# Performance work log

Hardware: AMD Instinct MI355X
Metric: run time of the kernel (lower is better)

The kernel has to match this reference:

```python
import jax, jax.numpy as jnp
import numpy as np

B = 8192        # number of drug-cell pairs (graphs)
NPG = 32        # nodes per graph
EPG = 64        # directed edges per graph
N = B * NPG     # total nodes
E = B * EPG     # total edges
CELL = 908      # cell_inp_dim
BN_EPS = 1e-5


def _bn(x):
    # BatchNorm1d in training mode with gamma=1, beta=0 (fresh init), biased var
    m = x.mean(0)
    v = x.var(0)
    return (x - m) * jax.lax.rsqrt(v + BN_EPS)


def _lin_params(k, fan_in, fan_out):
    kw, _ = jax.random.split(k)
    w = jax.random.normal(kw, (fan_in, fan_out), jnp.float32) / np.sqrt(fan_in)
    b = jnp.zeros((fan_out,), jnp.float32)
    return w, b


_DIMS = [("ce_1", CELL, 516), ("ce_2", 516, 256), ("ce_3", 256, 128),
         ("g1_1", 9, 128), ("g1_2", 128, 128),
         ("g2_1", 128, 128), ("g2_2", 128, 128),
         ("d_1", 128, 128), ("d_2", 128, 128),
         ("f_1", 256, 128), ("f_2", 128, 64), ("f_3", 64, 1)]


def setup_inputs() -> dict:
    key = jax.random.key(0)
    ks = jax.random.split(key, 4 + len(_DIMS))
    inp = {}
    inp["cell"] = jax.random.normal(ks[0], (B, CELL), jnp.float32)
    inp["drug_x"] = jax.random.normal(ks[1], (N, 9), jnp.float32)
    g = jnp.arange(E) // EPG  # graph id per edge
    src = g * NPG + jax.random.randint(ks[2], (E,), 0, NPG)
    dst = g * NPG + jax.random.randint(ks[3], (E,), 0, NPG)
    inp["drug_edge_index"] = jnp.stack([src, dst]).astype(jnp.int32)
    inp["drug_batch"] = (jnp.arange(N) // NPG).astype(jnp.int32)
    for i, (nm, a, b) in enumerate(_DIMS):
        w, bb = _lin_params(ks[4 + i], a, b)
        inp[nm + "_w"] = w
        inp[nm + "_b"] = bb
    return inp


def _forward(cell, drug_x, src, dst, batch,
             ce_1_w, ce_1_b, ce_2_w, ce_2_b, ce_3_w, ce_3_b,
             g1_1_w, g1_1_b, g1_2_w, g1_2_b,
             g2_1_w, g2_1_b, g2_2_w, g2_2_b,
             d_1_w, d_1_b, d_2_w, d_2_b,
             f_1_w, f_1_b, f_2_w, f_2_b, f_3_w, f_3_b):
    # cell_emb branch (dropout = identity in eval/reference)
    c = jax.nn.relu(_bn(cell @ ce_1_w + ce_1_b))
    c = jax.nn.relu(_bn(c @ ce_2_w + ce_2_b))
    c = jax.nn.relu(_bn(c @ ce_3_w + ce_3_b))

    # GINConv 1: h = MLP((1+eps)*x + sum_{j in N(i)} x_j), eps=0
    agg = jax.ops.segment_sum(drug_x[src], dst, num_segments=N)
    h = drug_x + agg
    h = jax.nn.relu(_bn(h @ g1_1_w + g1_1_b)) @ g1_2_w + g1_2_b  # inner MLP: Lin-BN-ReLU-Lin
    h = _bn(jax.nn.relu(h))  # outer ReLU then BN (per Sequential order)

    # GINConv 2
    agg = jax.ops.segment_sum(h[src], dst, num_segments=N)
    h = h + agg
    h = jax.nn.relu(_bn(h @ g2_1_w + g2_1_b)) @ g2_2_w + g2_2_b
    h = _bn(jax.nn.relu(h))

    # global max pool over nodes of each graph -> [B, 128]
    p = jax.ops.segment_max(h, batch, num_segments=B)

    d = jax.nn.relu(_bn(p @ d_1_w + d_1_b))
    d = jax.nn.relu(d @ d_2_w + d_2_b)

    z = jnp.concatenate([c, d], axis=-1)  # [B, 256]
    z = jax.nn.elu(_bn(z @ f_1_w + f_1_b))
    z = jax.nn.elu(_bn(z @ f_2_w + f_2_b))
    y = (z @ f_3_w + f_3_b).reshape(B)
    return y


def reference(cell, drug_x, drug_edge_index, drug_batch,
              ce_1_w, ce_1_b, ce_2_w, ce_2_b, ce_3_w, ce_3_b,
              g1_1_w, g1_1_b, g1_2_w, g1_2_b,
              g2_1_w, g2_1_b, g2_2_w, g2_2_b,
              d_1_w, d_1_b, d_2_w, d_2_b,
              f_1_w, f_1_b, f_2_w, f_2_b, f_3_w, f_3_b):
    src, dst = drug_edge_index[0], drug_edge_index[1]
    return _forward(cell, drug_x, src, dst, drug_batch,
                    ce_1_w, ce_1_b, ce_2_w, ce_2_b, ce_3_w, ce_3_b,
                    g1_1_w, g1_1_b, g1_2_w, g1_2_b,
                    g2_1_w, g2_1_b, g2_2_w, g2_2_b,
                    d_1_w, d_1_b, d_2_w, d_2_b,
                    f_1_w, f_1_b, f_2_w, f_2_b, f_3_w, f_3_b)
```

## Files before the change

kernel.cpp:

```cpp
#include <hip/hip_runtime.h>
#include <hip/hip_bf16.h>
#include <math.h>

#define BGRAPH 8192
#define NPG 32
#define EPG 64
#define NNODE (BGRAPH * NPG)
#define NEDGE (BGRAPH * EPG)
#define CELLD 908
#define BN_EPS 1e-5f
#define ABF_STR 960
#define C1_STR 576

typedef __attribute__((ext_vector_type(8))) short bf16x8;
typedef __attribute__((ext_vector_type(4))) float f32x4;
typedef __attribute__((ext_vector_type(4))) unsigned short us4;
typedef __attribute__((ext_vector_type(8))) unsigned short us8;

__device__ __forceinline__ unsigned short f2bf(float f)
{
    unsigned int u = __float_as_uint(f);
    u = (u + 0x7FFFu + ((u >> 16) & 1u)) >> 16;
    return (unsigned short)u;
}

__device__ __forceinline__ bf16x8 quant8(const float v[8])
{
    union { bf16x8 b; unsigned short u[8]; } fr;
    #pragma unroll
    for (int j = 0; j < 8; ++j) fr.u[j] = f2bf(v[j]);
    return fr.b;
}

__device__ __forceinline__ void bf2f8(bf16x8 b, float v[8])
{
    union { bf16x8 bb; unsigned short u[8]; } x; x.bb = b;
    #pragma unroll
    for (int j = 0; j < 8; ++j) v[j] = __uint_as_float((unsigned)x.u[j] << 16);
}

__device__ __forceinline__ float apply_in(float v, int mode, float mn, float iv)
{
    if (mode == 1)      { v = (v - mn) * iv; v = fmaxf(v, 0.f); }
    else if (mode == 2) { v = (v - mn) * iv; v = (v > 0.f) ? v : expm1f(v); }
    else if (mode == 3) { v = fmaxf(v, 0.f); v = (v - mn) * iv; }
    return v;
}

struct TransArgs {
    const float* w[11];
    unsigned short* wt[11];
    int K[11], N[11], ntN[11];
    int off[12];
};

__global__ void transpose_w(TransArgs a)
{
    __shared__ float t[64][65];
    int b = blockIdx.x, tid = threadIdx.x;
    int s = 0;
    while (s < 10 && b >= a.off[s + 1]) ++s;
    int t0 = b - a.off[s];
    int K = a.K[s], N = a.N[s], ntn = a.ntN[s];
    int kt = t0 / ntn, nt = t0 - kt * ntn;
    int k0 = kt * 64, n0 = nt * 64;
    const float* w = a.w[s];
    unsigned short* wt = a.wt[s];
    int c = tid & 63, rg = tid >> 6;
    #pragma unroll
    for (int i = 0; i < 16; ++i) {
        int rr = rg * 16 + i;
        int k = k0 + rr, n = n0 + c;
        t[c][rr] = (k < K && n < N) ? w[(size_t)k * N + n] : 0.f;
    }
    __syncthreads();
    #pragma unroll
    for (int i = 0; i < 16; ++i) {
        int rr = rg * 16 + i;
        int n = n0 + rr, k = k0 + c;
        if (n < N && k < K) wt[(size_t)n * K + k] = f2bf(t[rr][c]);
    }
}

struct SetupArgs {
    float* zb; int zTotal; int zBlocks;
    const int* src; const int* dst; int* row_start; int* col_idx;
};

__global__ void setup_all(SetupArgs a)
{
    int b = blockIdx.x;
    int tid = threadIdx.x;
    if (b < a.zBlocks) {
        int i = b * 256 + tid;
        if (i < a.zTotal) a.zb[i] = 0.f;
        return;
    }
    b -= a.zBlocks;
    __shared__ int cnt[4][32], fill[4][32], rsl[4][33];
    int gl = tid >> 6, e = tid & 63;
    int g = b * 4 + gl;
    if (e < 32) { cnt[gl][e] = 0; fill[gl][e] = 0; }
    __syncthreads();
    int s = a.src[g * EPG + e] - g * NPG;
    int d = a.dst[g * EPG + e] - g * NPG;
    atomicAdd(&cnt[gl][d], 1);
    __syncthreads();
    if (e == 0) {
        int acc = 0;
        for (int i = 0; i < 32; ++i) { rsl[gl][i] = acc; acc += cnt[gl][i]; }
        rsl[gl][32] = acc;
    }
    __syncthreads();
    int pos = rsl[gl][d] + atomicAdd(&fill[gl][d], 1);
    a.col_idx[g * EPG + pos] = s;
    if (e < 33) a.row_start[g * 33 + e] = rsl[gl][e];
}

__global__ void quant_cell(const float* __restrict__ cell, unsigned short* __restrict__ abf)
{
    int i = blockIdx.x * 256 + threadIdx.x;
    int row = i / (ABF_STR / 4), c4 = i - row * (ABF_STR / 4);
    int k = c4 * 4;
    us4 w = (us4){0, 0, 0, 0};
    if (k < CELLD) {
        float4 f = *(const float4*)&cell[(size_t)row * CELLD + k];
        w = (us4){ f2bf(f.x), f2bf(f.y), f2bf(f.z), f2bf(f.w) };
    }
    *(us4*)&abf[(size_t)row * ABF_STR + k] = w;
}

__global__ void quant_c1(const float* __restrict__ c1, const float* __restrict__ stats,
                         float inv_sM, unsigned short* __restrict__ out)
{
    int i = blockIdx.x * 256 + threadIdx.x;
    int row = i / (C1_STR / 4), c4 = i - row * (C1_STR / 4);
    int k = c4 * 4;
    us4 w = (us4){0, 0, 0, 0};
    if (k < 516) {
        float4 f = *(const float4*)&c1[(size_t)row * 516 + k];
        float v[4] = {f.x, f.y, f.z, f.w};
        #pragma unroll
        for (int j = 0; j < 4; ++j) {
            float s = stats[k + j], ss = stats[516 + k + j];
            float mn = s * inv_sM;
            float iv = rsqrtf(ss * inv_sM - mn * mn + BN_EPS);
            v[j] = fmaxf((v[j] - mn) * iv, 0.f);
        }
        w = (us4){ f2bf(v[0]), f2bf(v[1]), f2bf(v[2]), f2bf(v[3]) };
    }
    *(us4*)&out[(size_t)row * C1_STR + k] = w;
}

__global__ void reduce_stats(const float* __restrict__ part, int nrows,
                             float* __restrict__ out)
{
    int c = threadIdx.x;
    int per = nrows >> 6;
    int r0 = blockIdx.x * per;
    float s = 0.f;
    for (int r = 0; r < per; ++r) s += part[(size_t)(r0 + r) * 256 + c];
    unsafeAtomicAdd(&out[c], s);
}

#define HBS 136

__launch_bounds__(256)
__global__ void gin_s1(const float* __restrict__ drug_x,
                       const int* __restrict__ row_start,
                       const int* __restrict__ col_idx,
                       const unsigned short* __restrict__ W11,
                       const float* __restrict__ b11,
                       unsigned short* uout,
                       float* __restrict__ part)
{
    __shared__ __align__(16) unsigned short h[4 * 32 * HBS];
    __shared__ __align__(16) unsigned char ubuf[4096];
    __shared__ int rs[4][36];
    __shared__ int ci[4][64];

    unsigned short* w11l = (unsigned short*)ubuf;
    float* red = (float*)ubuf;

    int tid  = threadIdx.x;
    int wave = tid >> 6;
    int lane = tid & 63;
    int quad = lane >> 4;
    int l16  = lane & 15;
    int g0   = blockIdx.x * 4;
    unsigned short* hw = h + wave * (32 * HBS);
    float* xw = (float*)hw;

    for (int i = tid; i < 128 * 16; i += 256) {
        int n = i >> 4, k = i & 15;
        w11l[i] = (k < 9) ? W11[n * 9 + k] : (unsigned short)0;
    }
    if (tid < 132) {
        int gl = tid / 33, idx = tid - gl * 33;
        rs[gl][idx] = row_start[(g0 + gl) * 33 + idx];
    }
    {
        int gl = tid >> 6, e = tid & 63;
        ci[gl][e] = col_idx[(g0 + gl) * EPG + e];
    }
    {
        const float* xg = drug_x + (size_t)(g0 + wave) * 32 * 9;
        for (int i = lane; i < 32 * 16; i += 64) {
            int rr = i >> 4, c = i & 15;
            xw[i] = (c < 9) ? xg[rr * 9 + c] : 0.f;
        }
    }
    __syncthreads();

    f32x4 acc[2][8];
    #pragma unroll
    for (int i = 0; i < 2; ++i)
        #pragma unroll
        for (int j = 0; j < 8; ++j)
            acc[i][j] = (f32x4){0.f, 0.f, 0.f, 0.f};

    {
        bf16x8 af[2];
        #pragma unroll
        for (int mt = 0; mt < 2; ++mt) {
            int rowl = mt * 16 + l16;
            float v[8] = {0, 0, 0, 0, 0, 0, 0, 0};
            if (quad < 2) {
                float4 lo = *(const float4*)&xw[rowl * 16 + quad * 8];
                float4 hi = *(const float4*)&xw[rowl * 16 + quad * 8 + 4];
                v[0] = lo.x; v[1] = lo.y; v[2] = lo.z; v[3] = lo.w;
                v[4] = hi.x; v[5] = hi.y; v[6] = hi.z; v[7] = hi.w;
                int e0 = rs[wave][rowl], e1 = rs[wave][rowl + 1];
                for (int e = e0; e < e1; ++e) {
                    int sr = ci[wave][e];
                    float4 l2 = *(const float4*)&xw[sr * 16 + quad * 8];
                    float4 h2 = *(const float4*)&xw[sr * 16 + quad * 8 + 4];
                    v[0] += l2.x; v[1] += l2.y; v[2] += l2.z; v[3] += l2.w;
                    v[4] += h2.x; v[5] += h2.y; v[6] += h2.z; v[7] += h2.w;
                }
            }
            af[mt] = quant8(v);
        }
        #pragma unroll
        for (int nt = 0; nt < 8; ++nt) {
            bf16x8 b;
            if (quad < 2) b = *(const bf16x8*)(const void*)&w11l[(nt * 16 + l16) * 16 + quad * 8];
            else { float z[8] = {0,0,0,0,0,0,0,0}; b = quant8(z); }
            acc[0][nt] = __builtin_amdgcn_mfma_f32_16x16x32_bf16(af[0], b, acc[0][nt], 0, 0, 0);
            acc[1][nt] = __builtin_amdgcn_mfma_f32_16x16x32_bf16(af[1], b, acc[1][nt], 0, 0, 0);
        }
    }

    float ls[8], lq[8];
    unsigned short* ub = uout + (size_t)(g0 + wave) * 32 * 128;
    #pragma unroll
    for (int nt = 0; nt < 8; ++nt) {
        int col = nt * 16 + l16;
        float bv = b11[col];
        float s0 = 0.f, q0 = 0.f;
        #pragma unroll
        for (int mt = 0; mt < 2; ++mt) {
            int rb = mt * 16 + quad * 4;
            #pragma unroll
            for (int r = 0; r < 4; ++r) {
                float u = acc[mt][nt][r] + bv;
                ub[(size_t)(rb + r) * 128 + col] = f2bf(u);
                s0 += u; q0 += u * u;
            }
        }
        ls[nt] = s0; lq[nt] = q0;
    }
    __syncthreads();
    #pragma unroll
    for (int nt = 0; nt < 8; ++nt) {
        float s = ls[nt], q = lq[nt];
        s += __shfl_xor(s, 16); q += __shfl_xor(q, 16);
        s += __shfl_xor(s, 32); q += __shfl_xor(q, 32);
        if (quad == 0) {
            int col = nt * 16 + l16;
            red[(wave * 2 + 0) * 128 + col] = s;
            red[(wave * 2 + 1) * 128 + col] = q;
        }
    }
    __syncthreads();
    if (tid < 128) {
        float s = red[0 * 128 + tid] + red[2 * 128 + tid] + red[4 * 128 + tid] + red[6 * 128 + tid];
        float q = red[1 * 128 + tid] + red[3 * 128 + tid] + red[5 * 128 + tid] + red[7 * 128 + tid];
        part[(size_t)blockIdx.x * 256 + tid] = s;
        part[(size_t)blockIdx.x * 256 + 128 + tid] = q;
    }
}

__launch_bounds__(256)
__global__ void gin_s3f(const unsigned short* __restrict__ uin,
                        const int* __restrict__ row_start,
                        const int* __restrict__ col_idx,
                        const unsigned short* __restrict__ Wt,
                        const float* __restrict__ bias,
                        const float* __restrict__ in_stats, float inv_sM,
                        unsigned short* __restrict__ uout,
                        float* __restrict__ part)
{
    __shared__ __align__(16) unsigned short wsl[128 * 136];
    __shared__ float pmv[256];
    __shared__ int rs[2][33];
    __shared__ int ci[2][64];
    float* zt = (float*)wsl;

    int tid  = threadIdx.x;
    int wave = tid >> 6;
    int lane = tid & 63;
    int quad = lane >> 4;
    int l16  = lane & 15;
    int g0   = blockIdx.x * 2;
    int row0 = blockIdx.x * 64;

    if (tid < 128) {
        float s = in_stats[tid], ss = in_stats[128 + tid];
        float mn = s * inv_sM;
        pmv[tid] = mn;
        pmv[128 + tid] = rsqrtf(ss * inv_sM - mn * mn + BN_EPS);
    }
    if (tid < 66) {
        int gl = tid / 33, idx = tid - gl * 33;
        rs[gl][idx] = row_start[(g0 + gl) * 33 + idx];
    }
    if (tid >= 128) {
        int t = tid - 128;
        ci[t >> 6][t & 63] = col_idx[(g0 + (t >> 6)) * EPG + (t & 63)];
    }
    for (int i = tid; i < 128 * 32; i += 256) {
        int n = i >> 5, k = (i & 31) * 4;
        *(us4*)&wsl[n * 136 + k] = *(const us4*)&Wt[(size_t)n * 128 + k];
    }
    __syncthreads();

    bf16x8 afrag[4];
    {
        const unsigned short* ap = uin + (size_t)(row0 + wave * 16 + l16) * 128;
        #pragma unroll
        for (int ks = 0; ks < 4; ++ks) {
            int kb = ks * 32 + quad * 8;
            float v[8];
            bf2f8(*(const bf16x8*)(const void*)&ap[kb], v);
            #pragma unroll
            for (int j = 0; j < 8; ++j)
                v[j] = (fmaxf(v[j], 0.f) - pmv[kb + j]) * pmv[128 + kb + j];
            afrag[ks] = quant8(v);
        }
    }

    f32x4 acc[8];
    #pragma unroll
    for (int j = 0; j < 8; ++j) acc[j] = (f32x4){0.f, 0.f, 0.f, 0.f};
    #pragma unroll
    for (int ks = 0; ks < 4; ++ks) {
        int kb = ks * 32 + quad * 8;
        #pragma unroll
        for (int nt = 0; nt < 8; ++nt) {
            bf16x8 b = *(const bf16x8*)(const void*)&wsl[(nt * 16 + l16) * 136 + kb];
            acc[nt] = __builtin_amdgcn_mfma_f32_16x16x32_bf16(afrag[ks], b, acc[nt], 0, 0, 0);
        }
    }
    __syncthreads();

    #pragma unroll
    for (int nt = 0; nt < 8; ++nt) {
        int col = nt * 16 + l16;
        #pragma unroll
        for (int r = 0; r < 4; ++r)
            zt[(wave * 16 + quad * 4 + r) * 132 + col] = acc[nt][r];
    }
    __syncthreads();

    float sv[4] = {0.f, 0.f, 0.f, 0.f}, qv[4] = {0.f, 0.f, 0.f, 0.f};
    {
        int c4  = (tid & 31) * 4;
        int rg  = tid >> 5;
        int hh  = rg >> 2;
        int rb0 = (rg & 3) * 8;
        float4 bv = *(const float4*)&bias[c4];
        unsigned short* ub = uout + (size_t)row0 * 128;
        for (int rr = 0; rr < 8; ++rr) {
            int r = rb0 + rr;
            int lr = hh * 32 + r;
            float4 val = *(const float4*)&zt[lr * 132 + c4];
            int e0 = rs[hh][r], e1 = rs[hh][r + 1];
            for (int e = e0; e < e1; ++e) {
                float4 zz = *(const float4*)&zt[(hh * 32 + ci[hh][e]) * 132 + c4];
                val.x += zz.x; val.y += zz.y; val.z += zz.z; val.w += zz.w;
            }
            float u0 = val.x + bv.x, u1 = val.y + bv.y;
            float u2 = val.z + bv.z, u3 = val.w + bv.w;
            *(us4*)&ub[(size_t)lr * 128 + c4] =
                (us4){ f2bf(u0), f2bf(u1), f2bf(u2), f2bf(u3) };
            sv[0] += u0; sv[1] += u1; sv[2] += u2; sv[3] += u3;
            qv[0] += u0 * u0; qv[1] += u1 * u1; qv[2] += u2 * u2; qv[3] += u3 * u3;
        }
    }
    __syncthreads();
    {
        int c4 = (tid & 31) * 4, rg = tid >> 5;
        #pragma unroll
        for (int j = 0; j < 4; ++j) {
            zt[rg * 128 + c4 + j] = sv[j];
            zt[1024 + rg * 128 + c4 + j] = qv[j];
        }
    }
    __syncthreads();
    if (tid < 128) {
        float s = 0.f, q = 0.f;
        #pragma unroll
        for (int rg = 0; rg < 8; ++rg) {
            s += zt[rg * 128 + tid];
            q += zt[1024 + rg * 128 + tid];
        }
        part[(size_t)blockIdx.x * 256 + tid] = s;
        part[(size_t)blockIdx.x * 256 + 128 + tid] = q;
    }
}

template<int DO_POOL>
__launch_bounds__(256)
__global__ void gin_lin(const unsigned short* __restrict__ uin,
                        const unsigned short* __restrict__ Wt,
                        const float* __restrict__ bias,
                        const float* __restrict__ in_stats, float inv_sM,
                        unsigned short* uout,
                        float* __restrict__ part,
                        float* __restrict__ pool_out)
{
    __shared__ __align__(16) unsigned short Ws_l[128 * 136];
    __shared__ float pmv[256];
    __shared__ float red[4][2][128];

    int tid  = threadIdx.x;
    int wave = tid >> 6;
    int lane = tid & 63;
    int quad = lane >> 4;
    int l16  = lane & 15;
    int row0 = blockIdx.x * 64;

    for (int i = tid; i < 128 * 32; i += 256) {
        int n = i >> 5, k = (i & 31) * 4;
        *(us4*)&Ws_l[n * 136 + k] = *(const us4*)&Wt[(size_t)n * 128 + k];
    }
    if (tid < 128) {
        float s = in_stats[tid], ss = in_stats[128 + tid];
        float mn = s * inv_sM;
        pmv[tid] = mn;
        pmv[128 + tid] = rsqrtf(ss * inv_sM - mn * mn + BN_EPS);
    }
    __syncthreads();

    bf16x8 afrag[4];
    {
        const unsigned short* ap = uin + (size_t)(row0 + wave * 16 + l16) * 128;
        #pragma unroll
        for (int ks = 0; ks < 4; ++ks) {
            int kb = ks * 32 + quad * 8;
            float v[8];
            bf2f8(*(const bf16x8*)(const void*)&ap[kb], v);
            #pragma unroll
            for (int j = 0; j < 8; ++j)
                v[j] = fmaxf((v[j] - pmv[kb + j]) * pmv[128 + kb + j], 0.f);
            afrag[ks] = quant8(v);
        }
    }

    f32x4 acc[8];
    #pragma unroll
    for (int j = 0; j < 8; ++j) acc[j] = (f32x4){0.f, 0.f, 0.f, 0.f};
    #pragma unroll
    for (int ks = 0; ks < 4; ++ks) {
        int kb = ks * 32 + quad * 8;
        #pragma unroll
        for (int nt = 0; nt < 8; ++nt) {
            bf16x8 b = *(const bf16x8*)(const void*)&Ws_l[(nt * 16 + l16) * 136 + kb];
            acc[nt] = __builtin_amdgcn_mfma_f32_16x16x32_bf16(afrag[ks], b, acc[nt], 0, 0, 0);
        }
    }

    float ls[8], lq[8], lm[8];
    #pragma unroll
    for (int nt = 0; nt < 8; ++nt) {
        int col = nt * 16 + l16;
        float bv = bias[col];
        int rb = row0 + wave * 16 + quad * 4;
        float s0 = 0.f, q0 = 0.f, mx = -INFINITY;
        #pragma unroll
        for (int r = 0; r < 4; ++r) {
            float u = acc[nt][r] + bv;
            float ru = fmaxf(u, 0.f);
            s0 += ru; q0 += ru * ru;
            if (DO_POOL) mx = fmaxf(mx, ru);
            else uout[(size_t)(rb + r) * 128 + col] = f2bf(u);
        }
        ls[nt] = s0; lq[nt] = q0; lm[nt] = mx;
    }

    #pragma unroll
    for (int nt = 0; nt < 8; ++nt) {
        float s = ls[nt], q = lq[nt];
        s += __shfl_xor(s, 16); q += __shfl_xor(q, 16);
        s += __shfl_xor(s, 32); q += __shfl_xor(q, 32);
        if (quad == 0) {
            red[wave][0][nt * 16 + l16] = s;
            red[wave][1][nt * 16 + l16] = q;
        }
    }
    __syncthreads();
    if (tid < 128) {
        float s = red[0][0][tid] + red[1][0][tid] + red[2][0][tid] + red[3][0][tid];
        float q = red[0][1][tid] + red[1][1][tid] + red[2][1][tid] + red[3][1][tid];
        part[(size_t)blockIdx.x * 256 + tid] = s;
        part[(size_t)blockIdx.x * 256 + 128 + tid] = q;
    }
    if (DO_POOL) {
        __syncthreads();
        #pragma unroll
        for (int nt = 0; nt < 8; ++nt) {
            float m = lm[nt];
            m = fmaxf(m, __shfl_xor(m, 16));
            m = fmaxf(m, __shfl_xor(m, 32));
            if (quad == 0) red[wave][0][nt * 16 + l16] = m;
        }
        __syncthreads();
        {
            int gi = tid >> 7, col = tid & 127;
            float m = fmaxf(red[gi * 2][0][col], red[gi * 2 + 1][0][col]);
            pool_out[(size_t)((row0 >> 5) + gi) * 128 + col] = m;
        }
    }
}

template<int KSTEPS, int NT>
__launch_bounds__(256)
__global__ void gemm_rA(const float* __restrict__ A, const float* __restrict__ A2,
                        int lda, int K, int stats_K, int ksplit,
                        const unsigned short* __restrict__ Wt,
                        const float* __restrict__ bias, float* __restrict__ C,
                        const float* __restrict__ in_stats, float inv_sM, int in_mode,
                        float* __restrict__ out_stats, int stats_mode, int out_act)
{
    constexpr int LSTRW = KSTEPS * 32 + 8;
    constexpr int NSUB = NT / 16;
    __shared__ unsigned short Ws_l[NT * LSTRW];
    __shared__ float pm[KSTEPS * 32], pv[KSTEPS * 32];
    __shared__ float red[4][2][NT];

    int tid  = threadIdx.x;
    int wave = tid >> 6;
    int lane = tid & 63;
    int quad = lane >> 4;
    int l16  = lane & 15;
    int m0   = blockIdx.x * 64;

    const bool kvec = ((K & 3) == 0);

    for (int i = tid; i < NT * (KSTEPS * 8); i += 256) {
        int n = i / (KSTEPS * 8), g4 = i % (KSTEPS * 8);
        int k = g4 * 4;
        us4 w = (us4){0, 0, 0, 0};
        if (k < K) {
            const unsigned short* wp = Wt + (size_t)n * K + k;
            if (kvec) w = *(const us4*)wp;
            else {
                w.x = wp[0];
                if (k + 1 < K) w.y = wp[1];
                if (k + 2 < K) w.z = wp[2];
                if (k + 3 < K) w.w = wp[3];
            }
        }
        *(us4*)&Ws_l[n * LSTRW + k] = w;
    }
    if (in_mode) {
        for (int k = tid; k < KSTEPS * 32; k += 256) {
            float mn = 0.f, iv = 1.f;
            if (k < stats_K) {
                float s = in_stats[k], ss = in_stats[stats_K + k];
                mn = s * inv_sM;
                float vr = ss * inv_sM - mn * mn;
                iv = rsqrtf(vr + BN_EPS);
            }
            pm[k] = mn; pv[k] = iv;
        }
    }
    __syncthreads();

    bf16x8 afrag[KSTEPS];
    {
        int row = m0 + wave * 16 + l16;
        const float* ap = A + (size_t)row * lda;
        #pragma unroll
        for (int ks = 0; ks < KSTEPS; ++ks) {
            int kb = ks * 32 + quad * 8;
            float v[8];
            if (kvec) {
                #pragma unroll
                for (int hh = 0; hh < 2; ++hh) {
                    int k = kb + hh * 4;
                    const float* p = (k >= ksplit) ? &A2[(size_t)row * 128 + (k - 128)]
                                                   : &ap[k];
                    float4 f = *(const float4*)p;
                    v[hh * 4 + 0] = f.x; v[hh * 4 + 1] = f.y;
                    v[hh * 4 + 2] = f.z; v[hh * 4 + 3] = f.w;
                }
            } else {
                #pragma unroll
                for (int j = 0; j < 8; ++j) {
                    int k = kb + j;
                    v[j] = (k < K) ? ap[k] : 0.f;
                }
            }
            if (in_mode) {
                #pragma unroll
                for (int j = 0; j < 8; ++j)
                    v[j] = apply_in(v[j], in_mode, pm[kb + j], pv[kb + j]);
            }
            afrag[ks] = quant8(v);
        }
    }

    f32x4 acc[NSUB];
    #pragma unroll
    for (int j = 0; j < NSUB; ++j) acc[j] = (f32x4){0.f, 0.f, 0.f, 0.f};

    #pragma unroll
    for (int ks = 0; ks < KSTEPS; ++ks) {
        #pragma unroll
        for (int nt = 0; nt < NSUB; ++nt) {
            bf16x8 b = *(const bf16x8*)(const void*)&Ws_l[(nt * 16 + l16) * LSTRW + ks * 32 + quad * 8];
            acc[nt] = __builtin_amdgcn_mfma_f32_16x16x32_bf16(afrag[ks], b, acc[nt], 0, 0, 0);
        }
    }

    float ls[NSUB], lq[NSUB];
    #pragma unroll
    for (int nt = 0; nt < NSUB; ++nt) { ls[nt] = 0.f; lq[nt] = 0.f; }

    #pragma unroll
    for (int nt = 0; nt < NSUB; ++nt) {
        int col = nt * 16 + l16;
        float bv = bias[col];
        int rbase = m0 + wave * 16 + quad * 4;
        #pragma unroll
        for (int r = 0; r < 4; ++r) {
            float u = acc[nt][r] + bv;
            if (C) {
                float wv = out_act ? fmaxf(u, 0.f) : u;
                C[(size_t)(rbase + r) * NT + col] = wv;
            }
            if (stats_mode) {
                float s = (stats_mode == 2) ? fmaxf(u, 0.f) : u;
                ls[nt] += s; lq[nt] += s * s;
            }
        }
    }

    if (stats_mode) {
        #pragma unroll
        for (int nt = 0; nt < NSUB; ++nt) {
            float s = ls[nt], q = lq[nt];
            s += __shfl_xor(s, 16); q += __shfl_xor(q, 16);
            s += __shfl_xor(s, 32); q += __shfl_xor(q, 32);
            if (quad == 0) { red[wave][0][nt * 16 + l16] = s; red[wave][1][nt * 16 + l16] = q; }
        }
        __syncthreads();
        if (tid < NT) {
            float s = red[0][0][tid] + red[1][0][tid] + red[2][0][tid] + red[3][0][tid];
            float q = red[0][1][tid] + red[1][1][tid] + red[2][1][tid] + red[3][1][tid];
            unsafeAtomicAdd(&out_stats[tid], s);
            unsafeAtomicAdd(&out_stats[NT + tid], q);
        }
    }
}

template<int NT, int ABF>
__launch_bounds__(256)
__global__ void gemm_cell(const float* __restrict__ A,
                          const unsigned short* __restrict__ Abf, int abf_str,
                          const unsigned short* __restrict__ Wt,
                          const float* __restrict__ bias, float* __restrict__ C,
                          int M, int K, int N,
                          const float* __restrict__ in_stats, float inv_sM, int in_mode,
                          float* __restrict__ out_stats)
{
    constexpr int NSUB = NT / 16;
    constexpr int PMSZ = ABF ? 1 : 916;
    __shared__ unsigned short As_l[64 * 72];
    __shared__ unsigned short Ws_l[NT * 72];
    __shared__ float pm[PMSZ], pv[PMSZ];
    __shared__ float red[4][2][NT];

    int tid = threadIdx.x;
    int wave = tid >> 6;
    int lane = tid & 63;
    int quad = lane >> 4;
    int l16 = lane & 15;
    int m0 = blockIdx.x * 64, n0 = blockIdx.y * NT;

    if (!ABF && in_mode) {
        for (int k = tid; k < K; k += 256) {
            float s = in_stats[k], ss = in_stats[K + k];
            float mn = s * inv_sM;
            float vr = ss * inv_sM - mn * mn;
            pm[k] = mn; pv[k] = rsqrtf(vr + BN_EPS);
        }
        __syncthreads();
    }

    f32x4 acc[NSUB];
    #pragma unroll
    for (int j = 0; j < NSUB; ++j) acc[j] = (f32x4){0.f, 0.f, 0.f, 0.f};

    for (int k0 = 0; k0 < K; k0 += 64) {
        if (ABF) {
            #pragma unroll
            for (int t = 0; t < 2; ++t) {
                int i = t * 256 + tid;
                int row = i >> 3, c8 = (i & 7) * 8;
                us8 w = *(const us8*)&Abf[(size_t)(m0 + row) * abf_str + k0 + c8];
                *(us8*)&As_l[row * 72 + c8] = w;
            }
        } else {
            for (int i = tid; i < 64 * 16; i += 256) {
                int row = i >> 4, f4 = i & 15;
                int k = k0 + f4 * 4;
                us4 w4 = (us4){0, 0, 0, 0};
                if (k < K) {
                    float4 f = *(const float4*)&A[(size_t)(m0 + row) * K + k];
                    if (in_mode) {
                        f.x = apply_in(f.x, in_mode, pm[k], pv[k]);
                        f.y = apply_in(f.y, in_mode, pm[k + 1], pv[k + 1]);
                        f.z = apply_in(f.z, in_mode, pm[k + 2], pv[k + 2]);
                        f.w = apply_in(f.w, in_mode, pm[k + 3], pv[k + 3]);
                    }
                    w4 = (us4){ f2bf(f.x), f2bf(f.y), f2bf(f.z), f2bf(f.w) };
                }
                *(us4*)&As_l[row * 72 + f4 * 4] = w4;
            }
        }
        for (int i = tid; i < NT * 16; i += 256) {
            int nn = i >> 4, kt = i & 15;
            int k = k0 + kt * 4;
            int gn = n0 + nn;
            us4 w4 = (us4){0, 0, 0, 0};
            if (gn < N && k < K) w4 = *(const us4*)&Wt[(size_t)gn * K + k];
            *(us4*)&Ws_l[nn * 72 + kt * 4] = w4;
        }
        __syncthreads();
        int rowb = wave * 16;
        #pragma unroll
        for (int ks = 0; ks < 2; ++ks) {
            bf16x8 a = *(const bf16x8*)(const void*)&As_l[(rowb + l16) * 72 + ks * 32 + quad * 8];
            #pragma unroll
            for (int nt = 0; nt < NSUB; ++nt) {
                bf16x8 b = *(const bf16x8*)(const void*)&Ws_l[(nt * 16 + l16) * 72 + ks * 32 + quad * 8];
                acc[nt] = __builtin_amdgcn_mfma_f32_16x16x32_bf16(a, b, acc[nt], 0, 0, 0);
            }
        }
        __syncthreads();
    }

    float ls[NSUB], lq[NSUB];
    #pragma unroll
    for (int nt = 0; nt < NSUB; ++nt) { ls[nt] = 0.f; lq[nt] = 0.f; }

    #pragma unroll
    for (int nt = 0; nt < NSUB; ++nt) {
        int col = n0 + nt * 16 + l16;
        if (col < N) {
            float bv = bias[col];
            int rbase = m0 + wave * 16 + quad * 4;
            #pragma unroll
            for (int r = 0; r < 4; ++r) {
                float u = acc[nt][r] + bv;
                C[(size_t)(rbase + r) * N + col] = u;
                ls[nt] += u; lq[nt] += u * u;
            }
        }
    }

    #pragma unroll
    for (int nt = 0; nt < NSUB; ++nt) {
        float s = ls[nt], q = lq[nt];
        s += __shfl_xor(s, 16); q += __shfl_xor(q, 16);
        s += __shfl_xor(s, 32); q += __shfl_xor(q, 32);
        if (quad == 0) { red[wave][0][nt * 16 + l16] = s; red[wave][1][nt * 16 + l16] = q; }
    }
    __syncthreads();
    if (tid < NT) {
        int col = n0 + tid;
        if (col < N) {
            float s = red[0][0][tid] + red[1][0][tid] + red[2][0][tid] + red[3][0][tid];
            float q = red[0][1][tid] + red[1][1][tid] + red[2][1][tid] + red[3][1][tid];
            unsafeAtomicAdd(&out_stats[col], s);
            unsafeAtomicAdd(&out_stats[N + col], q);
        }
    }
}

__global__ void final_dot(const float* __restrict__ u, const float* __restrict__ w,
                          const float* __restrict__ b, float* __restrict__ y,
                          const float* __restrict__ stats, float inv_sM)
{
    __shared__ float pmv[64], piv[64], sw[64];
    int tid = threadIdx.x;
    if (tid < 64) {
        float s = stats[tid], ss = stats[64 + tid];
        float mn = s * inv_sM;
        float vr = ss * inv_sM - mn * mn;
        pmv[tid] = mn;
        piv[tid] = rsqrtf(vr + BN_EPS);
        sw[tid] = w[tid];
    }
    __syncthreads();
    int i = blockIdx.x * blockDim.x + tid;
    if (i >= BGRAPH) return;
    float acc = 0.f;
    #pragma unroll
    for (int k = 0; k < 64; ++k) {
        float v = (u[(size_t)i * 64 + k] - pmv[k]) * piv[k];
        v = (v > 0.f) ? v : expm1f(v);
        acc += v * sw[k];
    }
    y[i] = acc + b[0];
}

extern "C" void kernel_launch(void* const* d_in, const int* in_sizes, int n_in,
                              void* d_out, int out_size, void* d_ws, size_t ws_size,
                              hipStream_t stream)
{
    const float* cell   = (const float*)d_in[0];
    const float* drug_x = (const float*)d_in[1];
    const int*   eidx   = (const int*)d_in[2];
    const float* ce1w = (const float*)d_in[4];  const float* ce1b = (const float*)d_in[5];
    const float* ce2w = (const float*)d_in[6];  const float* ce2b = (const float*)d_in[7];
    const float* ce3w = (const float*)d_in[8];  const float* ce3b = (const float*)d_in[9];
    const float* g11w = (const float*)d_in[10]; const float* g11b = (const float*)d_in[11];
    const float* g12w = (const float*)d_in[12]; const float* g12b = (const float*)d_in[13];
    const float* g21w = (const float*)d_in[14]; const float* g21b = (const float*)d_in[15];
    const float* g22w = (const float*)d_in[16]; const float* g22b = (const float*)d_in[17];
    const float* d1w  = (const float*)d_in[18]; const float* d1b  = (const float*)d_in[19];
    const float* d2w  = (const float*)d_in[20]; const float* d2b  = (const float*)d_in[21];
    const float* f1w  = (const float*)d_in[22]; const float* f1b  = (const float*)d_in[23];
    const float* f2w  = (const float*)d_in[24]; const float* f2b  = (const float*)d_in[25];
    const float* f3w  = (const float*)d_in[26]; const float* f3b  = (const float*)d_in[27];

    const int* src = eidx;
    const int* dst = eidx + NEDGE;
    float* out = (float*)d_out;

    const float INV_N = 1.f / (float)NNODE;
    const float INV_B = 1.f / (float)BGRAPH;
    const int KBIG = 1 << 30;

    float* ws = (float*)d_ws;
    unsigned short* ubg = (unsigned short*)ws;
    float* pbuf = ws + (size_t)NNODE * 64;
    float* sb   = pbuf + (size_t)BGRAPH * 128;
    unsigned short* wtb = (unsigned short*)(sb + 10 * 1032);
    auto ST = [&](int i) { return sb + (size_t)i * 1032; };
    float* st_u1    = ST(0);
    float* st_u2rel = ST(1);
    float* st_u3    = ST(2);
    float* st_u4rel = ST(3);
    float* st_c1    = ST(4);
    float* st_c2    = ST(5);
    float* st_c3    = ST(6);
    float* st_d1    = ST(7);
    float* st_f1    = ST(8);
    float* st_f2    = ST(9);

    float* c1    = ws;
    float* c2    = c1 + (size_t)BGRAPH * 516;
    float* c3u   = c2 + (size_t)BGRAPH * 256;
    float* dbuf  = c3u + (size_t)BGRAPH * 128;
    float* d2buf = dbuf + (size_t)BGRAPH * 128;
    float* f1o   = d2buf + (size_t)BGRAPH * 128;
    float* f2o   = f1o + (size_t)BGRAPH * 128;

    struct WDef { const float* w; int K; int N; };
    WDef wd[11] = {
        {ce1w, CELLD, 516}, {ce2w, 516, 256}, {ce3w, 256, 128},
        {g11w, 9, 128}, {g12w, 128, 128}, {g21w, 128, 128}, {g22w, 128, 128},
        {d1w, 128, 128}, {d2w, 128, 128}, {f1w, 256, 128}, {f2w, 128, 64}
    };
    TransArgs ta;
    int off = 0;
    unsigned short* wt[11];
    ta.off[0] = 0;
    for (int i = 0; i < 11; ++i) {
        wt[i] = wtb + off;
        ta.w[i] = wd[i].w; ta.wt[i] = wt[i];
        ta.K[i] = wd[i].K; ta.N[i] = wd[i].N;
        ta.ntN[i] = (wd[i].N + 63) / 64;
        ta.off[i + 1] = ta.off[i] + ((wd[i].K + 63) / 64) * ta.ntN[i];
        off += wd[i].K * wd[i].N;
    }

    SetupArgs sa;
    sa.zb = sb; sa.zTotal = 10 * 1032; sa.zBlocks = (10 * 1032 + 255) / 256;
    sa.src = src; sa.dst = dst;

    int csr_off = (off + 7) & ~7;
    int* row_start = (int*)(wtb + csr_off);
    int* col_idx   = row_start + (size_t)BGRAPH * 33;
    float* part = (float*)(col_idx + (size_t)NEDGE);
    unsigned short* Abf  = (unsigned short*)(part + (size_t)4096 * 256);
    unsigned short* C1bf = Abf + (size_t)BGRAPH * ABF_STR;
    sa.row_start = row_start; sa.col_idx = col_idx;

    transpose_w<<<ta.off[11], 256, 0, stream>>>(ta);
    setup_all<<<sa.zBlocks + BGRAPH / 4, 256, 0, stream>>>(sa);

    gin_s1<<<BGRAPH / 4, 256, 0, stream>>>(
        drug_x, row_start, col_idx, wt[3], g11b, ubg, part);
    reduce_stats<<<64, 256, 0, stream>>>(part, BGRAPH / 4, st_u1);

    gin_lin<0><<<NNODE / 64, 256, 0, stream>>>(
        ubg, wt[4], g12b, st_u1, INV_N, ubg, part, nullptr);
    reduce_stats<<<64, 256, 0, stream>>>(part, NNODE / 64, st_u2rel);

    gin_s3f<<<BGRAPH / 2, 256, 0, stream>>>(
        ubg, row_start, col_idx, wt[5], g21b, st_u2rel, INV_N, ubg, part);
    reduce_stats<<<64, 256, 0, stream>>>(part, BGRAPH / 2, st_u3);

    gin_lin<1><<<NNODE / 64, 256, 0, stream>>>(
        ubg, wt[6], g22b, st_u3, INV_N, nullptr, part, pbuf);
    reduce_stats<<<64, 256, 0, stream>>>(part, NNODE / 64, st_u4rel);

    quant_cell<<<(BGRAPH * (ABF_STR / 4)) / 256, 256, 0, stream>>>(cell, Abf);
    gemm_cell<128, 1><<<dim3(BGRAPH / 64, 5), 256, 0, stream>>>(
        nullptr, Abf, ABF_STR, wt[0], ce1b, c1, BGRAPH, CELLD, 516,
        nullptr, 0.f, 0, st_c1);
    quant_c1<<<(BGRAPH * (C1_STR / 4)) / 256, 256, 0, stream>>>(c1, st_c1, INV_B, C1bf);
    gemm_cell<64, 1><<<dim3(BGRAPH / 64, 4), 256, 0, stream>>>(
        nullptr, C1bf, C1_STR, wt[1], ce2b, c2, BGRAPH, 516, 256,
        nullptr, 0.f, 0, st_c2);
    gemm_rA<8, 128><<<BGRAPH / 64, 256, 0, stream>>>(
        c2, nullptr, 256, 256, 256, KBIG, wt[2], ce3b, c3u,
        st_c2, INV_B, 1, st_c3, 1, 0);

    gemm_rA<4, 128><<<BGRAPH / 64, 256, 0, stream>>>(
        pbuf, nullptr, 128, 128, 128, KBIG, wt[7], d1b, dbuf,
        st_u4rel, INV_N, 3, st_d1, 1, 0);
    gemm_rA<4, 128><<<BGRAPH / 64, 256, 0, stream>>>(
        dbuf, nullptr, 128, 128, 128, KBIG, wt[8], d2b, d2buf,
        st_d1, INV_B, 1, nullptr, 0, 1);

    gemm_rA<8, 128><<<BGRAPH / 64, 256, 0, stream>>>(
        c3u, d2buf, 128, 256, 128, 128, wt[9], f1b, f1o,
        st_c3, INV_B, 1, st_f1, 1, 0);
    gemm_rA<4, 64><<<BGRAPH / 64, 256, 0, stream>>>(
        f1o, nullptr, 128, 128, 128, KBIG, wt[10], f2b, f2o,
        st_f1, INV_B, 2, st_f2, 1, 0);
    final_dot<<<BGRAPH / 256, 256, 0, stream>>>(f2o, f3w, f3b, out, st_f2, INV_B);
}
```

Measured before the change: 578.8 us.

## Split small-GEMM tiles to 16 rows and reduce BN stats via partials

The small dense GEMMs (cell layer 3, drug MLP, fusion layers) now give each block 16 rows instead of 64, with the four waves splitting the output columns. This quadruples the grid so more CUs get work. Per-block BatchNorm statistics are no longer combined in LDS and added with global atomics. They are written to a partial buffer and summed by extra reduce_stats launches, which now take a column count so 64-wide outputs work. The cost is four times more weight staging into LDS per row and several extra kernel launches.

```diff
diff --git a/kernel.cpp b/kernel.cpp
--- a/kernel.cpp
+++ b/kernel.cpp
@@ -152,15 +152,18 @@
     *(us4*)&out[(size_t)row * C1_STR + k] = w;
 }
 
-__global__ void reduce_stats(const float* __restrict__ part, int nrows,
+__global__ void reduce_stats(const float* __restrict__ part, int nrows, int nt,
                              float* __restrict__ out)
 {
     int c = threadIdx.x;
     int per = nrows >> 6;
     int r0 = blockIdx.x * per;
+    bool isq = (c >= 128);
+    int cc = isq ? c - 128 : c;
+    if (cc >= nt) return;
     float s = 0.f;
     for (int r = 0; r < per; ++r) s += part[(size_t)(r0 + r) * 256 + c];
-    unsafeAtomicAdd(&out[c], s);
+    unsafeAtomicAdd(&out[(isq ? nt : 0) + cc], s);
 }
 
 #define HBS 136
@@ -536,42 +539,30 @@
 
 template<int KSTEPS, int NT>
 __launch_bounds__(256)
-__global__ void gemm_rA(const float* __restrict__ A, const float* __restrict__ A2,
+__global__ void gemm_rB(const float* __restrict__ A, const float* __restrict__ A2,
                         int lda, int K, int stats_K, int ksplit,
                         const unsigned short* __restrict__ Wt,
                         const float* __restrict__ bias, float* __restrict__ C,
                         const float* __restrict__ in_stats, float inv_sM, int in_mode,
-                        float* __restrict__ out_stats, int stats_mode, int out_act)
+                        float* __restrict__ part, int stats_mode, int out_act)
 {
     constexpr int LSTRW = KSTEPS * 32 + 8;
-    constexpr int NSUB = NT / 16;
+    constexpr int NSUBW = NT / 64;
     __shared__ unsigned short Ws_l[NT * LSTRW];
     __shared__ float pm[KSTEPS * 32], pv[KSTEPS * 32];
-    __shared__ float red[4][2][NT];
 
     int tid  = threadIdx.x;
     int wave = tid >> 6;
     int lane = tid & 63;
     int quad = lane >> 4;
     int l16  = lane & 15;
-    int m0   = blockIdx.x * 64;
-
-    const bool kvec = ((K & 3) == 0);
+    int m0   = blockIdx.x * 16;
 
     for (int i = tid; i < NT * (KSTEPS * 8); i += 256) {
         int n = i / (KSTEPS * 8), g4 = i % (KSTEPS * 8);
         int k = g4 * 4;
         us4 w = (us4){0, 0, 0, 0};
-        if (k < K) {
-            const unsigned short* wp = Wt + (size_t)n * K + k;
-            if (kvec) w = *(const us4*)wp;
-            else {
-                w.x = wp[0];
-                if (k + 1 < K) w.y = wp[1];
-                if (k + 2 < K) w.z = wp[2];
-                if (k + 3 < K) w.w = wp[3];
-            }
-        }
+        if (k < K) w = *(const us4*)(Wt + (size_t)n * K + k);
         *(us4*)&Ws_l[n * LSTRW + k] = w;
     }
     if (in_mode) {
@@ -590,28 +581,20 @@
 
     bf16x8 afrag[KSTEPS];
     {
-        int row = m0 + wave * 16 + l16;
+        int row = m0 + l16;
         const float* ap = A + (size_t)row * lda;
         #pragma unroll
         for (int ks = 0; ks < KSTEPS; ++ks) {
             int kb = ks * 32 + quad * 8;
             float v[8];
-            if (kvec) {
-                #pragma unroll
-                for (int hh = 0; hh < 2; ++hh) {
-                    int k = kb + hh * 4;
-                    const float* p = (k >= ksplit) ? &A2[(size_t)row * 128 + (k - 128)]
-                                                   : &ap[k];
-                    float4 f = *(const float4*)p;
-                    v[hh * 4 + 0] = f.x; v[hh * 4 + 1] = f.y;
-                    v[hh * 4 + 2] = f.z; v[hh * 4 + 3] = f.w;
-                }
-            } else {
-                #pragma unroll
-                for (int j = 0; j < 8; ++j) {
-                    int k = kb + j;
-                    v[j] = (k < K) ? ap[k] : 0.f;
-                }
+            #pragma unroll
+            for (int hh = 0; hh < 2; ++hh) {
+                int k = kb + hh * 4;
+                const float* p = (k >= ksplit) ? &A2[(size_t)row * 128 + (k - 128)]
+                                               : &ap[k];
+                float4 f = *(const float4*)p;
+                v[hh * 4 + 0] = f.x; v[hh * 4 + 1] = f.y;
+                v[hh * 4 + 2] = f.z; v[hh * 4 + 3] = f.w;
             }
             if (in_mode) {
                 #pragma unroll
@@ -622,28 +605,29 @@
         }
     }
 
-    f32x4 acc[NSUB];
-    #pragma unroll
-    for (int j = 0; j < NSUB; ++j) acc[j] = (f32x4){0.f, 0.f, 0.f, 0.f};
+    f32x4 acc[NSUBW];
+    #pragma unroll
+    for (int j = 0; j < NSUBW; ++j) acc[j] = (f32x4){0.f, 0.f, 0.f, 0.f};
 
     #pragma unroll
     for (int ks = 0; ks < KSTEPS; ++ks) {
         #pragma unroll
-        for (int nt = 0; nt < NSUB; ++nt) {
-            bf16x8 b = *(const bf16x8*)(const void*)&Ws_l[(nt * 16 + l16) * LSTRW + ks * 32 + quad * 8];
+        for (int nt = 0; nt < NSUBW; ++nt) {
+            bf16x8 b = *(const bf16x8*)(const void*)
+                &Ws_l[((wave * NSUBW + nt) * 16 + l16) * LSTRW + ks * 32 + quad * 8];
             acc[nt] = __builtin_amdgcn_mfma_f32_16x16x32_bf16(afrag[ks], b, acc[nt], 0, 0, 0);
         }
     }
 
-    float ls[NSUB], lq[NSUB];
-    #pragma unroll
-    for (int nt = 0; nt < NSUB; ++nt) { ls[nt] = 0.f; lq[nt] = 0.f; }
-
-    #pragma unroll
-    for (int nt = 0; nt < NSUB; ++nt) {
-        int col = nt * 16 + l16;
+    float ls[NSUBW], lq[NSUBW];
+    #pragma unroll
+    for (int nt = 0; nt < NSUBW; ++nt) { ls[nt] = 0.f; lq[nt] = 0.f; }
+
+    #pragma unroll
+    for (int nt = 0; nt < NSUBW; ++nt) {
+        int col = (wave * NSUBW + nt) * 16 + l16;
         float bv = bias[col];
-        int rbase = m0 + wave * 16 + quad * 4;
+        int rbase = m0 + quad * 4;
         #pragma unroll
         for (int r = 0; r < 4; ++r) {
             float u = acc[nt][r] + bv;
@@ -660,18 +644,15 @@
 
     if (stats_mode) {
         #pragma unroll
-        for (int nt = 0; nt < NSUB; ++nt) {
+        for (int nt = 0; nt < NSUBW; ++nt) {
             float s = ls[nt], q = lq[nt];
             s += __shfl_xor(s, 16); q += __shfl_xor(q, 16);
             s += __shfl_xor(s, 32); q += __shfl_xor(q, 32);
-            if (quad == 0) { red[wave][0][nt * 16 + l16] = s; red[wave][1][nt * 16 + l16] = q; }
-        }
-        __syncthreads();
-        if (tid < NT) {
-            float s = red[0][0][tid] + red[1][0][tid] + red[2][0][tid] + red[3][0][tid];
-            float q = red[0][1][tid] + red[1][1][tid] + red[2][1][tid] + red[3][1][tid];
-            unsafeAtomicAdd(&out_stats[tid], s);
-            unsafeAtomicAdd(&out_stats[NT + tid], q);
+            if (quad == 0) {
+                int col = (wave * NSUBW + nt) * 16 + l16;
+                part[(size_t)blockIdx.x * 256 + col] = s;
+                part[(size_t)blockIdx.x * 256 + 128 + col] = q;
+            }
         }
     }
 }
@@ -917,19 +898,19 @@
 
     gin_s1<<<BGRAPH / 4, 256, 0, stream>>>(
         drug_x, row_start, col_idx, wt[3], g11b, ubg, part);
-    reduce_stats<<<64, 256, 0, stream>>>(part, BGRAPH / 4, st_u1);
+    reduce_stats<<<64, 256, 0, stream>>>(part, BGRAPH / 4, 128, st_u1);
 
     gin_lin<0><<<NNODE / 64, 256, 0, stream>>>(
         ubg, wt[4], g12b, st_u1, INV_N, ubg, part, nullptr);
-    reduce_stats<<<64, 256, 0, stream>>>(part, NNODE / 64, st_u2rel);
+    reduce_stats<<<64, 256, 0, stream>>>(part, NNODE / 64, 128, st_u2rel);
 
     gin_s3f<<<BGRAPH / 2, 256, 0, stream>>>(
         ubg, row_start, col_idx, wt[5], g21b, st_u2rel, INV_N, ubg, part);
-    reduce_stats<<<64, 256, 0, stream>>>(part, BGRAPH / 2, st_u3);
+    reduce_stats<<<64, 256, 0, stream>>>(part, BGRAPH / 2, 128, st_u3);
 
     gin_lin<1><<<NNODE / 64, 256, 0, stream>>>(
         ubg, wt[6], g22b, st_u3, INV_N, nullptr, part, pbuf);
-    reduce_stats<<<64, 256, 0, stream>>>(part, NNODE / 64, st_u4rel);
+    reduce_stats<<<64, 256, 0, stream>>>(part, NNODE / 64, 128, st_u4rel);
 
     quant_cell<<<(BGRAPH * (ABF_STR / 4)) / 256, 256, 0, stream>>>(cell, Abf);
     gemm_cell<128, 1><<<dim3(BGRAPH / 64, 5), 256, 0, stream>>>(
@@ -939,22 +920,26 @@
     gemm_cell<64, 1><<<dim3(BGRAPH / 64, 4), 256, 0, stream>>>(
         nullptr, C1bf, C1_STR, wt[1], ce2b, c2, BGRAPH, 516, 256,
         nullptr, 0.f, 0, st_c2);
-    gemm_rA<8, 128><<<BGRAPH / 64, 256, 0, stream>>>(
+    gemm_rB<8, 128><<<BGRAPH / 16, 256, 0, stream>>>(
         c2, nullptr, 256, 256, 256, KBIG, wt[2], ce3b, c3u,
-        st_c2, INV_B, 1, st_c3, 1, 0);
-
-    gemm_rA<4, 128><<<BGRAPH / 64, 256, 0, stream>>>(
+        st_c2, INV_B, 1, part, 1, 0);
+    reduce_stats<<<64, 256, 0, stream>>>(part, BGRAPH / 16, 128, st_c3);
+
+    gemm_rB<4, 128><<<BGRAPH / 16, 256, 0, stream>>>(
         pbuf, nullptr, 128, 128, 128, KBIG, wt[7], d1b, dbuf,
-        st_u4rel, INV_N, 3, st_d1, 1, 0);
-    gemm_rA<4, 128><<<BGRAPH / 64, 256, 0, stream>>>(
+        st_u4rel, INV_N, 3, part, 1, 0);
+    reduce_stats<<<64, 256, 0, stream>>>(part, BGRAPH / 16, 128, st_d1);
+    gemm_rB<4, 128><<<BGRAPH / 16, 256, 0, stream>>>(
         dbuf, nullptr, 128, 128, 128, KBIG, wt[8], d2b, d2buf,
-        st_d1, INV_B, 1, nullptr, 0, 1);
-
-    gemm_rA<8, 128><<<BGRAPH / 64, 256, 0, stream>>>(
+        st_d1, INV_B, 1, part, 0, 1);
+
+    gemm_rB<8, 128><<<BGRAPH / 16, 256, 0, stream>>>(
         c3u, d2buf, 128, 256, 128, 128, wt[9], f1b, f1o,
-        st_c3, INV_B, 1, st_f1, 1, 0);
-    gemm_rA<4, 64><<<BGRAPH / 64, 256, 0, stream>>>(
+        st_c3, INV_B, 1, part, 1, 0);
+    reduce_stats<<<64, 256, 0, stream>>>(part, BGRAPH / 16, 128, st_f1);
+    gemm_rB<4, 64><<<BGRAPH / 16, 256, 0, stream>>>(
         f1o, nullptr, 128, 128, 128, KBIG, wt[10], f2b, f2o,
-        st_f1, INV_B, 2, st_f2, 1, 0);
+        st_f1, INV_B, 2, part, 1, 0);
+    reduce_stats<<<64, 256, 0, stream>>>(part, BGRAPH / 16, 64, st_f2);
     final_dot<<<BGRAPH / 256, 256, 0, stream>>>(f2o, f3w, f3b, out, st_f2, INV_B);
 }
```

Result: faster. 567.1 us (-2.0%).
